# Performance work log

Measured on AMD Instinct MI355X. Metric: run time of the kernel, lower is better.

## Reference

```python
import jax, jax.numpy as jnp
import numpy as np

B, T, H = 64, 256, 128

def setup_inputs() -> dict:
    key = jax.random.key(0)
    ks = jax.random.split(key, 10)
    s = 1.0 / np.sqrt(H)
    return {
        "x": jax.random.normal(ks[0], (B, T, 2), jnp.float32),
        "enc_output": jax.random.normal(ks[1], (B, T, H), jnp.float32),
        "h0": jax.random.normal(ks[2], (B, H), jnp.float32) * s,
        "c0": jax.random.normal(ks[3], (B, H), jnp.float32) * s,
        "W1": jax.random.normal(ks[4], (H, H), jnp.float32) * s,
        "W2": jax.random.normal(ks[5], (H, H), jnp.float32) * s,
        "V": jax.random.normal(ks[6], (H,), jnp.float32) * s,
        "Wk": jax.random.normal(ks[7], (2, 4 * H), jnp.float32) * (1.0 / np.sqrt(2.0)),
        "Wr": jax.random.normal(ks[8], (H, 4 * H), jnp.float32) * s,
        "b": jnp.zeros((4 * H,), jnp.float32),
    }


def reference(x, enc_output, h0, c0, W1, W2, V, Wk, Wr, b):
    Bb, Tt, _ = x.shape
    # Precompute W1 @ enc_output once (original recomputes it T times inside K.rnn)
    enc_proj = jnp.einsum('bth,hk->btk', enc_output, W1)  # [B,T,H]

    def lstm_cell(inp, h, c):
        # Keras LSTMCell, gate order i,f,c,o; sigmoid recurrent activation, tanh activation
        z = inp @ Wk + h @ Wr + b  # [B,4H]
        zi, zf, zg, zo = jnp.split(z, 4, axis=-1)
        i = jax.nn.sigmoid(zi)
        f = jax.nn.sigmoid(zf)
        g = jnp.tanh(zg)
        o = jax.nn.sigmoid(zo)
        c_new = f * c + i * g
        h_new = o * jnp.tanh(c_new)
        return h_new, c_new

    def step(carry, _):
        h, c, ptr = carry
        h, c = lstm_cell(ptr, h, c)
        # additive attention over all encoder steps, batched (replaces inner K.rnn)
        scores = jnp.einsum('btk,k->bt', jnp.tanh(enc_proj + (h @ W2)[:, None, :]), V)
        probs = jax.nn.softmax(scores, axis=1)  # [B,T]
        # get_pointer with rank=0: top-1 of descending argsort == argmax
        idx = jnp.argmax(probs, axis=1)  # [B]
        ptr = jnp.take_along_axis(x, idx[:, None, None], axis=1)[:, 0, :]  # [B,2]
        return (h, c, ptr), probs

    ptr0 = jnp.ones((Bb, 2), x.dtype)
    _, probs_seq = jax.lax.scan(step, (h0, c0, ptr0), None, length=Tt)  # [T,B,T]
    return jnp.transpose(probs_seq, (1, 0, 2))  # [B,T,T]
```

## Files before the change

### kernel.cpp

```cpp
#include <hip/hip_runtime.h>
#include <cstddef>

#define TT 256
#define HH 128
#define EST 132

__device__ __forceinline__ float rdlane(float v, int l) {
  return __int_as_float(__builtin_amdgcn_readlane(__float_as_int(v), l));
}
__device__ __forceinline__ float fast_sigmoid(float x) {
  const float L2E = 1.4426950408889634f;
  float y = __builtin_amdgcn_exp2f(-x * L2E);
  return __builtin_amdgcn_rcpf(1.0f + y);
}
__device__ __forceinline__ float fast_tanh(float x) {
  const float C2 = 2.8853900817779268f;
  float y = __builtin_amdgcn_exp2f(x * C2);
  return 1.0f - 2.0f * __builtin_amdgcn_rcpf(1.0f + y);
}

__global__ __launch_bounds__(512, 2)
void decoder_kernel(const float* __restrict__ x,
                    const float* __restrict__ enc_output,
                    const float* __restrict__ h0,
                    const float* __restrict__ c0,
                    const float* __restrict__ W1,
                    const float* __restrict__ W2,
                    const float* __restrict__ V,
                    const float* __restrict__ Wk,
                    const float* __restrict__ Wr,
                    const float* __restrict__ bias,
                    float* __restrict__ out)
{
  __shared__ float E[TT * EST];
  __shared__ float zpart[4 * 512];
  __shared__ float part[8][64];
  __shared__ float scp[8 * 257];
  __shared__ float hbuf[HH];
  __shared__ float xloc[TT * 2];
  __shared__ float amax_s[4];
  __shared__ int   amax_t[4];
  __shared__ float ssum[4];

  const int u    = threadIdx.x;
  const int b    = blockIdx.x;
  const int lane = u & 63;
  const int w    = u >> 6;
  const float C2  = 2.8853900817779268f;
  const float L2E = 1.4426950408889634f;

  {
    const float* encb = enc_output + (size_t)b * TT * HH;
    const int tsub = u >> 4;
    const int ks   = (u & 15) * 8;
    for (int p = 0; p < 8; ++p) {
      const int tt = p * 32 + tsub;
      float4 a0 = {0.f, 0.f, 0.f, 0.f};
      float4 a1 = {0.f, 0.f, 0.f, 0.f};
      const float4* er4 = (const float4*)(encb + tt * HH);
      for (int j4 = 0; j4 < 32; ++j4) {
        const float4 ev = er4[j4];
        const float* w1p = W1 + (j4 * 4) * HH + ks;
        float4 wa, wb;
        wa = *(const float4*)(w1p + 0 * HH); wb = *(const float4*)(w1p + 0 * HH + 4);
        a0.x += ev.x * wa.x; a0.y += ev.x * wa.y; a0.z += ev.x * wa.z; a0.w += ev.x * wa.w;
        a1.x += ev.x * wb.x; a1.y += ev.x * wb.y; a1.z += ev.x * wb.z; a1.w += ev.x * wb.w;
        wa = *(const float4*)(w1p + 1 * HH); wb = *(const float4*)(w1p + 1 * HH + 4);
        a0.x += ev.y * wa.x; a0.y += ev.y * wa.y; a0.z += ev.y * wa.z; a0.w += ev.y * wa.w;
        a1.x += ev.y * wb.x; a1.y += ev.y * wb.y; a1.z += ev.y * wb.z; a1.w += ev.y * wb.w;
        wa = *(const float4*)(w1p + 2 * HH); wb = *(const float4*)(w1p + 2 * HH + 4);
        a0.x += ev.z * wa.x; a0.y += ev.z * wa.y; a0.z += ev.z * wa.z; a0.w += ev.z * wa.w;
        a1.x += ev.z * wb.x; a1.y += ev.z * wb.y; a1.z += ev.z * wb.z; a1.w += ev.z * wb.w;
        wa = *(const float4*)(w1p + 3 * HH); wb = *(const float4*)(w1p + 3 * HH + 4);
        a0.x += ev.w * wa.x; a0.y += ev.w * wa.y; a0.z += ev.w * wa.z; a0.w += ev.w * wa.w;
        a1.x += ev.w * wb.x; a1.y += ev.w * wb.y; a1.z += ev.w * wb.z; a1.w += ev.w * wb.w;
      }
      *(float4*)(&E[tt * EST + ks])     = a0;
      *(float4*)(&E[tt * EST + ks + 4]) = a1;
    }
  }
  xloc[u] = x[b * (TT * 2) + u];
  if (u < HH) hbuf[u] = h0[b * HH + u];

  const int kq = u >> 7;
  const int cs = u & 127;
  float4 wr4[32];
  #pragma unroll
  for (int i = 0; i < 32; ++i)
    wr4[i] = *(const float4*)(Wr + (32 * kq + i) * 512 + 4 * cs);
  const int g = u & 3;
  const int m = u >> 2;
  const int col = g * HH + m;
  const float wk0 = Wk[col];
  const float wk1 = Wk[512 + col];
  const float bb  = bias[col];
  const int halfC = w & 1;
  const int tqC   = w >> 1;
  float w2col[32];
  #pragma unroll
  for (int jj = 0; jj < 32; ++jj)
    w2col[jj] = W2[(32 * tqC + jj) * HH + 64 * halfC + lane];
  const int kstar = 16 * w + (lane & 15);
  const int pD    = kstar >> 6;
  const int lD    = kstar & 63;
  const float v2r = -2.0f * V[kstar];
  float c = c0[b * HH + m];
  float ptr0 = 1.0f, ptr1 = 1.0f;
  float svr;
  {
    float v = V[lane] + V[64 + lane];
    #pragma unroll
    for (int o = 1; o < 64; o <<= 1) v += __shfl_xor(v, o, 64);
    svr = v;
  }

  __syncthreads();

  {
    float* Er = &E[(u >> 1) * EST + 64 * (u & 1)];
    #pragma unroll
    for (int i = 0; i < 16; ++i) {
      float4 ev = *(const float4*)(Er + 4 * i);
      ev.x = __builtin_amdgcn_exp2f(ev.x * C2);
      ev.y = __builtin_amdgcn_exp2f(ev.y * C2);
      ev.z = __builtin_amdgcn_exp2f(ev.z * C2);
      ev.w = __builtin_amdgcn_exp2f(ev.w * C2);
      *(float4*)(Er + 4 * i) = ev;
    }
  }
  float hA = hbuf[32 * kq + (lane & 31)];
  float hC = hbuf[32 * tqC + (lane & 31)];
  __syncthreads();

  float* outb = out + (size_t)b * TT * TT;

  #pragma unroll 1
  for (int step = 0; step < TT; ++step) {
    {
      float4 zac = {0.f, 0.f, 0.f, 0.f};
      #pragma unroll
      for (int i = 0; i < 32; ++i) {
        float hi = rdlane(hA, i);
        zac.x += hi * wr4[i].x;
        zac.y += hi * wr4[i].y;
        zac.z += hi * wr4[i].z;
        zac.w += hi * wr4[i].w;
      }
      *(float4*)(&zpart[kq * 512 + 4 * cs]) = zac;
    }
    __syncthreads();

    {
      float z = bb + ptr0 * wk0 + ptr1 * wk1;
      z += (zpart[0 * 512 + col] + zpart[1 * 512 + col]) +
           (zpart[2 * 512 + col] + zpart[3 * 512 + col]);
      float za = __shfl_xor(z, 1);
      float zb = __shfl_xor(z, 2);
      float zc = __shfl_xor(za, 2);
      float zi = (g == 0) ? z  : (g == 1) ? za : (g == 2) ? zb : zc;
      float zf = (g == 0) ? za : (g == 1) ? z  : (g == 2) ? zc : zb;
      float zg = (g == 0) ? zb : (g == 1) ? zc : (g == 2) ? z  : za;
      float zo = (g == 0) ? zc : (g == 1) ? zb : (g == 2) ? za : z;
      float ig = fast_sigmoid(zi);
      float fg = fast_sigmoid(zf);
      float gg = fast_tanh(zg);
      float og = fast_sigmoid(zo);
      c = fg * c + ig * gg;
      float hn = og * fast_tanh(c);
      if (g == 0) hbuf[m] = hn;
    }
    __syncthreads();
    hA = hbuf[32 * kq + (lane & 31)];
    hC = hbuf[32 * tqC + (lane & 31)];

    {
      float cp0 = 0.0f, cp1 = 0.0f;
      #pragma unroll
      for (int jj = 0; jj < 32; jj += 2) {
        cp0 += rdlane(hC, jj)     * w2col[jj];
        cp1 += rdlane(hC, jj + 1) * w2col[jj + 1];
      }
      part[w][lane] = cp0 + cp1;
    }
    __syncthreads();

    float Uk;
    {
      float usum = (part[pD][lD] + part[pD + 2][lD]) +
                   (part[pD + 4][lD] + part[pD + 6][lD]);
      Uk = __builtin_amdgcn_exp2f(usum * C2);
    }

    {
      float uL[16], vL[16];
      #pragma unroll
      for (int i = 0; i < 16; ++i) {
        uL[i] = rdlane(Uk, i);
        vL[i] = rdlane(v2r, i);
      }
      #pragma unroll
      for (int tt = 0; tt < 4; ++tt) {
        const float* Er = &E[(64 * tt + lane) * EST + 16 * w];
        float4 e0 = *(const float4*)(Er + 0);
        float4 e1 = *(const float4*)(Er + 4);
        float4 e2 = *(const float4*)(Er + 8);
        float4 e3 = *(const float4*)(Er + 12);
        float a0 = 0.0f, a1 = 0.0f;
        a0 += vL[ 0] * __builtin_amdgcn_rcpf(1.0f + e0.x * uL[ 0]);
        a1 += vL[ 1] * __builtin_amdgcn_rcpf(1.0f + e0.y * uL[ 1]);
        a0 += vL[ 2] * __builtin_amdgcn_rcpf(1.0f + e0.z * uL[ 2]);
        a1 += vL[ 3] * __builtin_amdgcn_rcpf(1.0f + e0.w * uL[ 3]);
        a0 += vL[ 4] * __builtin_amdgcn_rcpf(1.0f + e1.x * uL[ 4]);
        a1 += vL[ 5] * __builtin_amdgcn_rcpf(1.0f + e1.y * uL[ 5]);
        a0 += vL[ 6] * __builtin_amdgcn_rcpf(1.0f + e1.z * uL[ 6]);
        a1 += vL[ 7] * __builtin_amdgcn_rcpf(1.0f + e1.w * uL[ 7]);
        a0 += vL[ 8] * __builtin_amdgcn_rcpf(1.0f + e2.x * uL[ 8]);
        a1 += vL[ 9] * __builtin_amdgcn_rcpf(1.0f + e2.y * uL[ 9]);
        a0 += vL[10] * __builtin_amdgcn_rcpf(1.0f + e2.z * uL[10]);
        a1 += vL[11] * __builtin_amdgcn_rcpf(1.0f + e2.w * uL[11]);
        a0 += vL[12] * __builtin_amdgcn_rcpf(1.0f + e3.x * uL[12]);
        a1 += vL[13] * __builtin_amdgcn_rcpf(1.0f + e3.y * uL[13]);
        a0 += vL[14] * __builtin_amdgcn_rcpf(1.0f + e3.z * uL[14]);
        a1 += vL[15] * __builtin_amdgcn_rcpf(1.0f + e3.w * uL[15]);
        scp[w * 257 + 64 * tt + lane] = a0 + a1;
      }
    }
    __syncthreads();

    float p = 0.0f;
    if (u < 256) {
      float s0 = 0.0f, s1 = 0.0f;
      #pragma unroll
      for (int q = 0; q < 8; q += 2) {
        s0 += scp[q * 257 + u];
        s1 += scp[(q + 1) * 257 + u];
      }
      float score = svr + s0 + s1;
      p = __builtin_amdgcn_exp2f((score - 12.0f) * L2E);
      float mx = score;
      float wsv = p;
      #pragma unroll
      for (int o = 1; o < 64; o <<= 1) {
        mx = fmaxf(mx, __shfl_xor(mx, o));
        wsv += __shfl_xor(wsv, o);
      }
      unsigned long long bal = __ballot(score == mx);
      int bt = 64 * w + (__ffsll(bal) - 1);
      if (lane == 0) { amax_s[w] = mx; amax_t[w] = bt; ssum[w] = wsv; }
    }
    __syncthreads();

    float fbs = amax_s[0]; int fbt = amax_t[0];
    #pragma unroll
    for (int q = 1; q < 4; ++q) {
      float s2v = amax_s[q]; int t2v = amax_t[q];
      if (s2v > fbs || (s2v == fbs && t2v < fbt)) { fbs = s2v; fbt = t2v; }
    }
    float sumtot = (ssum[0] + ssum[1]) + (ssum[2] + ssum[3]);
    ptr0 = xloc[2 * fbt + 0];
    ptr1 = xloc[2 * fbt + 1];
    if (u < 256) outb[(size_t)step * TT + u] = p * __builtin_amdgcn_rcpf(sumtot);
  }
}

extern "C" void kernel_launch(void* const* d_in, const int* in_sizes, int n_in,
                              void* d_out, int out_size, void* d_ws, size_t ws_size,
                              hipStream_t stream) {
  (void)in_sizes; (void)n_in; (void)d_ws; (void)ws_size; (void)out_size;
  const float* x    = (const float*)d_in[0];
  const float* enc  = (const float*)d_in[1];
  const float* h0   = (const float*)d_in[2];
  const float* c0   = (const float*)d_in[3];
  const float* W1   = (const float*)d_in[4];
  const float* W2   = (const float*)d_in[5];
  const float* V    = (const float*)d_in[6];
  const float* Wk   = (const float*)d_in[7];
  const float* Wr   = (const float*)d_in[8];
  const float* bias = (const float*)d_in[9];
  float* out = (float*)d_out;

  decoder_kernel<<<64, 512, 0, stream>>>(x, enc, h0, c0, W1, W2, V, Wk, Wr, bias, out);
}
```

Before: 948.0 us.

## Move recurrent matvec before attention barrier, pair reciprocals, hoist V lanes

The h@Wr partial matvec for the next step is now computed right after the attention score pass and shares its barrier, which removes one __syncthreads per step. The first step's matvec moves to the prologue. The attention inner loop merges two rcp terms into one by forming a common denominator, halving transcendental rcp calls at the cost of extra FMAs and some overflow or precision risk for large products. The V lane broadcasts are hoisted out of the step loop, which raises register pressure.

Result: faster. 870.0 us (-8.2%).

```diff
diff --git a/kernel.cpp b/kernel.cpp
--- a/kernel.cpp
+++ b/kernel.cpp
@@ -128,28 +128,30 @@
       *(float4*)(Er + 4 * i) = ev;
     }
   }
+  float vL[16];
+  #pragma unroll
+  for (int i = 0; i < 16; ++i) vL[i] = rdlane(v2r, i);
+
   float hA = hbuf[32 * kq + (lane & 31)];
   float hC = hbuf[32 * tqC + (lane & 31)];
+  {
+    float4 zac = {0.f, 0.f, 0.f, 0.f};
+    #pragma unroll
+    for (int i = 0; i < 32; ++i) {
+      float hi = rdlane(hA, i);
+      zac.x += hi * wr4[i].x;
+      zac.y += hi * wr4[i].y;
+      zac.z += hi * wr4[i].z;
+      zac.w += hi * wr4[i].w;
+    }
+    *(float4*)(&zpart[kq * 512 + 4 * cs]) = zac;
+  }
   __syncthreads();
 
   float* outb = out + (size_t)b * TT * TT;
 
   #pragma unroll 1
   for (int step = 0; step < TT; ++step) {
-    {
-      float4 zac = {0.f, 0.f, 0.f, 0.f};
-      #pragma unroll
-      for (int i = 0; i < 32; ++i) {
-        float hi = rdlane(hA, i);
-        zac.x += hi * wr4[i].x;
-        zac.y += hi * wr4[i].y;
-        zac.z += hi * wr4[i].z;
-        zac.w += hi * wr4[i].w;
-      }
-      *(float4*)(&zpart[kq * 512 + 4 * cs]) = zac;
-    }
-    __syncthreads();
-
     {
       float z = bb + ptr0 * wk0 + ptr1 * wk1;
       z += (zpart[0 * 512 + col] + zpart[1 * 512 + col]) +
@@ -190,14 +192,10 @@
                    (part[pD + 4][lD] + part[pD + 6][lD]);
       Uk = __builtin_amdgcn_exp2f(usum * C2);
     }
-
-    {
-      float uL[16], vL[16];
-      #pragma unroll
-      for (int i = 0; i < 16; ++i) {
-        uL[i] = rdlane(Uk, i);
-        vL[i] = rdlane(v2r, i);
-      }
+    {
+      float uL[16];
+      #pragma unroll
+      for (int i = 0; i < 16; ++i) uL[i] = rdlane(Uk, i);
       #pragma unroll
       for (int tt = 0; tt < 4; ++tt) {
         const float* Er = &E[(64 * tt + lane) * EST + 16 * w];
@@ -206,24 +204,45 @@
         float4 e2 = *(const float4*)(Er + 8);
         float4 e3 = *(const float4*)(Er + 12);
         float a0 = 0.0f, a1 = 0.0f;
-        a0 += vL[ 0] * __builtin_amdgcn_rcpf(1.0f + e0.x * uL[ 0]);
-        a1 += vL[ 1] * __builtin_amdgcn_rcpf(1.0f + e0.y * uL[ 1]);
-        a0 += vL[ 2] * __builtin_amdgcn_rcpf(1.0f + e0.z * uL[ 2]);
-        a1 += vL[ 3] * __builtin_amdgcn_rcpf(1.0f + e0.w * uL[ 3]);
-        a0 += vL[ 4] * __builtin_amdgcn_rcpf(1.0f + e1.x * uL[ 4]);
-        a1 += vL[ 5] * __builtin_amdgcn_rcpf(1.0f + e1.y * uL[ 5]);
-        a0 += vL[ 6] * __builtin_amdgcn_rcpf(1.0f + e1.z * uL[ 6]);
-        a1 += vL[ 7] * __builtin_amdgcn_rcpf(1.0f + e1.w * uL[ 7]);
-        a0 += vL[ 8] * __builtin_amdgcn_rcpf(1.0f + e2.x * uL[ 8]);
-        a1 += vL[ 9] * __builtin_amdgcn_rcpf(1.0f + e2.y * uL[ 9]);
-        a0 += vL[10] * __builtin_amdgcn_rcpf(1.0f + e2.z * uL[10]);
-        a1 += vL[11] * __builtin_amdgcn_rcpf(1.0f + e2.w * uL[11]);
-        a0 += vL[12] * __builtin_amdgcn_rcpf(1.0f + e3.x * uL[12]);
-        a1 += vL[13] * __builtin_amdgcn_rcpf(1.0f + e3.y * uL[13]);
-        a0 += vL[14] * __builtin_amdgcn_rcpf(1.0f + e3.z * uL[14]);
-        a1 += vL[15] * __builtin_amdgcn_rcpf(1.0f + e3.w * uL[15]);
+        float t0, t1, n;
+        t0 = fmaf(e0.x, uL[ 0], 1.0f); t1 = fmaf(e0.y, uL[ 1], 1.0f);
+        n  = fmaf(vL[ 1], t0, vL[ 0] * t1);
+        a0 = fmaf(n, __builtin_amdgcn_rcpf(t0 * t1), a0);
+        t0 = fmaf(e0.z, uL[ 2], 1.0f); t1 = fmaf(e0.w, uL[ 3], 1.0f);
+        n  = fmaf(vL[ 3], t0, vL[ 2] * t1);
+        a1 = fmaf(n, __builtin_amdgcn_rcpf(t0 * t1), a1);
+        t0 = fmaf(e1.x, uL[ 4], 1.0f); t1 = fmaf(e1.y, uL[ 5], 1.0f);
+        n  = fmaf(vL[ 5], t0, vL[ 4] * t1);
+        a0 = fmaf(n, __builtin_amdgcn_rcpf(t0 * t1), a0);
+        t0 = fmaf(e1.z, uL[ 6], 1.0f); t1 = fmaf(e1.w, uL[ 7], 1.0f);
+        n  = fmaf(vL[ 7], t0, vL[ 6] * t1);
+        a1 = fmaf(n, __builtin_amdgcn_rcpf(t0 * t1), a1);
+        t0 = fmaf(e2.x, uL[ 8], 1.0f); t1 = fmaf(e2.y, uL[ 9], 1.0f);
+        n  = fmaf(vL[ 9], t0, vL[ 8] * t1);
+        a0 = fmaf(n, __builtin_amdgcn_rcpf(t0 * t1), a0);
+        t0 = fmaf(e2.z, uL[10], 1.0f); t1 = fmaf(e2.w, uL[11], 1.0f);
+        n  = fmaf(vL[11], t0, vL[10] * t1);
+        a1 = fmaf(n, __builtin_amdgcn_rcpf(t0 * t1), a1);
+        t0 = fmaf(e3.x, uL[12], 1.0f); t1 = fmaf(e3.y, uL[13], 1.0f);
+        n  = fmaf(vL[13], t0, vL[12] * t1);
+        a0 = fmaf(n, __builtin_amdgcn_rcpf(t0 * t1), a0);
+        t0 = fmaf(e3.z, uL[14], 1.0f); t1 = fmaf(e3.w, uL[15], 1.0f);
+        n  = fmaf(vL[15], t0, vL[14] * t1);
+        a1 = fmaf(n, __builtin_amdgcn_rcpf(t0 * t1), a1);
         scp[w * 257 + 64 * tt + lane] = a0 + a1;
       }
+    }
+    {
+      float4 zac = {0.f, 0.f, 0.f, 0.f};
+      #pragma unroll
+      for (int i = 0; i < 32; ++i) {
+        float hi = rdlane(hA, i);
+        zac.x += hi * wr4[i].x;
+        zac.y += hi * wr4[i].y;
+        zac.z += hi * wr4[i].z;
+        zac.w += hi * wr4[i].w;
+      }
+      *(float4*)(&zpart[kq * 512 + 4 * cs]) = zac;
     }
     __syncthreads();
 
```
